# Kernel tuning notes

Hardware: AMD Instinct MI355X
Metric: run time of the kernel (lower is better)

## Reference

```python
import jax, jax.numpy as jnp
import numpy as np

H = 16        # attention heads
TOP_K = 2     # experts per token
EPS = 1e-5


def _layer_norm(x, g, b):
    m = x.mean(-1, keepdims=True)
    v = ((x - m) ** 2).mean(-1, keepdims=True)
    return (x - m) * jax.lax.rsqrt(v + EPS) * g + b


def setup_inputs() -> dict:
    key = jax.random.key(0)
    ks = jax.random.split(key, 12)
    B, S, D, F, E = 8, 512, 1024, 4096, 8
    inp = {
        "x": jax.random.normal(ks[0], (B, S, D), jnp.float32),
        "ln1_g": jnp.ones((D,), jnp.float32),
        "ln1_b": jnp.zeros((D,), jnp.float32),
        "ln2_g": jnp.ones((D,), jnp.float32),
        "ln2_b": jnp.zeros((D,), jnp.float32),
        "w_qkv": jax.random.normal(ks[1], (D, 3 * D), jnp.float32) * (D ** -0.5),
        "w_o": jax.random.normal(ks[2], (D, D), jnp.float32) * (D ** -0.5),
        "w_gate": jax.random.normal(ks[3], (D, E), jnp.float32) * (D ** -0.5),
        "w1": jax.random.normal(ks[4], (E, D, F), jnp.float32) * (D ** -0.5),
        "b1": jnp.zeros((E, F), jnp.float32),
        "w2": jax.random.normal(ks[5], (E, F, D), jnp.float32) * (F ** -0.5),
        "b2": jnp.zeros((E, D), jnp.float32),
    }
    return inp


def _block(x, ln1_g, ln1_b, ln2_g, ln2_b, w_qkv, w_o, w_gate, w1, b1, w2, b2):
    B, S, D = x.shape
    hd = D // H
    # --- attention (causal MHA) ---
    h = _layer_norm(x, ln1_g, ln1_b)
    qkv = h @ w_qkv                                   # [B,S,3D]
    q, k, v = jnp.split(qkv, 3, axis=-1)
    q = q.reshape(B, S, H, hd)
    k = k.reshape(B, S, H, hd)
    v = v.reshape(B, S, H, hd)
    scores = jnp.einsum("bqhd,bkhd->bhqk", q, k) * (hd ** -0.5)
    causal = jnp.tril(jnp.ones((S, S), bool))
    scores = jnp.where(causal, scores, jnp.finfo(scores.dtype).min)
    attn = jax.nn.softmax(scores, axis=-1)
    o = jnp.einsum("bhqk,bkhd->bqhd", attn, v).reshape(B, S, D)
    x_resid = x + o @ w_o
    # --- MoE FFN (top-k routing; dispatch/expert/combine math) ---
    moe_in = _layer_norm(x_resid, ln2_g, ln2_b)
    N = B * S
    xf = moe_in.reshape(N, D)
    probs = jax.nn.softmax(xf @ w_gate, axis=-1)       # [N,E]
    top_w, top_i = jax.lax.top_k(probs, TOP_K)         # [N,K]
    top_w = top_w / top_w.sum(-1, keepdims=True)       # renormalize over chosen experts
    E = w1.shape[0]
    out = jnp.zeros_like(xf)
    for e in range(E):                                 # fixed small expert loop
        gate_e = jnp.sum(jnp.where(top_i == e, top_w, 0.0), axis=-1)  # [N] combine weight
        he = jax.nn.gelu(xf @ w1[e] + b1[e])           # [N,F]
        out = out + gate_e[:, None] * (he @ w2[e] + b2[e])
    return out.reshape(B, S, D) + x_resid


def reference(x, ln1_g, ln1_b, ln2_g, ln2_b, w_qkv, w_o, w_gate, w1, b1, w2, b2):
    return _block(x, ln1_g, ln1_b, ln2_g, ln2_b, w_qkv, w_o, w_gate, w1, b1, w2, b2)
```

## Files before the change

kernel.cpp:

```cpp
#include <hip/hip_runtime.h>

#define DEV static __device__ __forceinline__

typedef __bf16 bf16;
typedef __bf16 bf16x8 __attribute__((ext_vector_type(8)));
typedef float f32x4 __attribute__((ext_vector_type(4)));

static_assert(sizeof(bf16x8) == 16, "bf16x8 must be 16B");

DEV void gll16(const void* g, void* l) {
  __builtin_amdgcn_global_load_lds(
      (const __attribute__((address_space(1))) unsigned int*)g,
      (__attribute__((address_space(3))) unsigned int*)l, 16, 0, 0);
}

__global__ void transpose_cvt_kernel(const float* __restrict__ src, bf16* __restrict__ hi,
                                     bf16* __restrict__ lo, int R, int C) {
  __shared__ float t[32][33];
  const int z = blockIdx.z;
  const size_t zoff = (size_t)z * R * C;
  const int c0 = blockIdx.x * 32, r0 = blockIdx.y * 32;
  const int tid = threadIdx.x;
#pragma unroll
  for (int i = 0; i < 4; ++i) {
    int idx = tid + i * 256;
    int r = idx >> 5, c = idx & 31;
    t[r][c] = src[zoff + (size_t)(r0 + r) * C + (c0 + c)];
  }
  __syncthreads();
#pragma unroll
  for (int i = 0; i < 4; ++i) {
    int idx = tid + i * 256;
    int c = idx >> 5, r = idx & 31;
    float v = t[r][c];
    bf16 h = (bf16)v;
    size_t o = zoff + (size_t)(c0 + c) * R + (r0 + r);
    hi[o] = h;
    if (lo) lo[o] = (bf16)(v - (float)h);
  }
}

DEV void block_reduce2(float& a, float& b, float* red, int tid) {
#pragma unroll
  for (int m = 32; m >= 1; m >>= 1) {
    a += __shfl_xor(a, m);
    b += __shfl_xor(b, m);
  }
  if ((tid & 63) == 0) {
    red[(tid >> 6) * 2] = a;
    red[(tid >> 6) * 2 + 1] = b;
  }
  __syncthreads();
  a = red[0] + red[2] + red[4] + red[6];
  b = red[1] + red[3] + red[5] + red[7];
}

__global__ void ln_split_kernel(const float* __restrict__ x, const float* __restrict__ g,
                                const float* __restrict__ bb, bf16* __restrict__ hi,
                                bf16* __restrict__ lo) {
  __shared__ float red[8];
  const int n = blockIdx.x, tid = threadIdx.x;
  const float* row = x + (size_t)n * 1024;
  float4 v = *(const float4*)(row + tid * 4);
  float s = v.x + v.y + v.z + v.w;
  float ss = v.x * v.x + v.y * v.y + v.z * v.z + v.w * v.w;
  block_reduce2(s, ss, red, tid);
  float mean = s * (1.f / 1024.f);
  float var = ss * (1.f / 1024.f) - mean * mean;
  float rstd = rsqrtf(var + 1e-5f);
  float vv[4] = {v.x, v.y, v.z, v.w};
#pragma unroll
  for (int c = 0; c < 4; ++c) {
    int col = tid * 4 + c;
    float y = (vv[c] - mean) * rstd * g[col] + bb[col];
    bf16 h = (bf16)y;
    size_t o = (size_t)n * 1024 + col;
    hi[o] = h;
    lo[o] = (bf16)(y - (float)h);
  }
}

__global__ __launch_bounds__(256, 2) void gemm_x3_kernel(
    const bf16* __restrict__ Ah, const bf16* __restrict__ Al, const bf16* __restrict__ Bh,
    const bf16* __restrict__ Bl, const float* __restrict__ addend, float* __restrict__ C, int M,
    int N, int K) {
  __shared__ bf16 As_h[128 * 64];
  __shared__ bf16 As_l[128 * 64];
  __shared__ bf16 Bs_h[128 * 64];
  __shared__ bf16 Bs_l[128 * 64];
  const int tid = threadIdx.x;
  const int w = tid >> 6, lane = tid & 63;
  const int quad = lane >> 4, l15 = lane & 15;
  const int m0 = blockIdx.y * 128, n0 = blockIdx.x * 128;
  const int wm = (w >> 1) * 64, wn = (w & 1) * 64;
  const int r8 = lane >> 3, c8 = lane & 7;

  size_t gA[4], gB[4];
  unsigned lbase[4];
#pragma unroll
  for (int i = 0; i < 4; ++i) {
    int rr = ((w * 4 + i) << 3) + r8;
    gA[i] = (size_t)(m0 + rr) * K + (c8 << 3);
    gB[i] = (size_t)(n0 + rr) * K + (c8 << 3);
    lbase[i] = (unsigned)((w * 4 + i) << 9);
  }
  const f32x4 fz = {0.f, 0.f, 0.f, 0.f};
  f32x4 acc[4][4];
#pragma unroll
  for (int a = 0; a < 4; ++a)
#pragma unroll
    for (int b = 0; b < 4; ++b) acc[a][b] = fz;

  for (int k0 = 0; k0 < K; k0 += 64) {
#pragma unroll
    for (int i = 0; i < 4; ++i) {
      gll16(Ah + gA[i] + k0, As_h + lbase[i]);
      gll16(Al + gA[i] + k0, As_l + lbase[i]);
      gll16(Bh + gB[i] + k0, Bs_h + lbase[i]);
      gll16(Bl + gB[i] + k0, Bs_l + lbase[i]);
    }
    __syncthreads();
#pragma unroll
    for (int ks = 0; ks < 2; ++ks) {
      bf16x8 a_h[4], a_l[4], b_h[4], b_l[4];
#pragma unroll
      for (int mi = 0; mi < 4; ++mi) {
        int off = (wm + mi * 16 + l15) * 64 + ks * 32 + quad * 8;
        a_h[mi] = *(const bf16x8*)(As_h + off);
        a_l[mi] = *(const bf16x8*)(As_l + off);
      }
#pragma unroll
      for (int ni = 0; ni < 4; ++ni) {
        int off = (wn + ni * 16 + l15) * 64 + ks * 32 + quad * 8;
        b_h[ni] = *(const bf16x8*)(Bs_h + off);
        b_l[ni] = *(const bf16x8*)(Bs_l + off);
      }
#pragma unroll
      for (int mi = 0; mi < 4; ++mi)
#pragma unroll
        for (int ni = 0; ni < 4; ++ni) {
          acc[mi][ni] = __builtin_amdgcn_mfma_f32_16x16x32_bf16(a_h[mi], b_h[ni], acc[mi][ni], 0, 0, 0);
          acc[mi][ni] = __builtin_amdgcn_mfma_f32_16x16x32_bf16(a_h[mi], b_l[ni], acc[mi][ni], 0, 0, 0);
          acc[mi][ni] = __builtin_amdgcn_mfma_f32_16x16x32_bf16(a_l[mi], b_h[ni], acc[mi][ni], 0, 0, 0);
        }
    }
    __syncthreads();
  }
#pragma unroll
  for (int mi = 0; mi < 4; ++mi)
#pragma unroll
    for (int r = 0; r < 4; ++r) {
      int row = m0 + wm + mi * 16 + quad * 4 + r;
      size_t rb = (size_t)row * N;
#pragma unroll
      for (int ni = 0; ni < 4; ++ni) {
        int col = n0 + wn + ni * 16 + l15;
        float v = acc[mi][ni][r];
        if (addend) v += addend[rb + col];
        C[rb + col] = v;
      }
    }
}

__global__ __launch_bounds__(256) void attn_kernel(const float* __restrict__ qkv,
                                                   bf16* __restrict__ o_hi,
                                                   bf16* __restrict__ o_lo) {
  __shared__ float Ks[64][64];
  __shared__ float Vs[64][64];
  const int bh = blockIdx.x;
  const int b = bh >> 4, h = bh & 15;
  const int q0 = blockIdx.y * 64;
  const int tid = threadIdx.x;
  const int ql = tid >> 2, sub = tid & 3;
  const size_t rowq = (size_t)(b * 512 + q0 + ql) * 3072 + h * 64 + sub * 16;
  float q[16];
#pragma unroll
  for (int j = 0; j < 16; ++j) q[j] = qkv[rowq + j] * 0.125f;
  float m_i = -1e30f, l_i = 0.f;
  float o[16];
#pragma unroll
  for (int j = 0; j < 16; ++j) o[j] = 0.f;
  const int ntiles = blockIdx.y + 1;
  for (int t = 0; t < ntiles; ++t) {
    const int kv0 = t * 64;
    __syncthreads();
    for (int i = tid; i < 1024; i += 256) {
      int r = i >> 4, c4 = (i & 15) << 2;
      const float* kp = qkv + (size_t)(b * 512 + kv0 + r) * 3072 + 1024 + h * 64 + c4;
      *(float4*)&Ks[r][c4] = *(const float4*)kp;
      *(float4*)&Vs[r][c4] = *(const float4*)(kp + 1024);
    }
    __syncthreads();
    const int kvlim = min(64, q0 + ql - kv0 + 1);
    for (int kv = 0; kv < kvlim; ++kv) {
      float s = 0.f;
#pragma unroll
      for (int j = 0; j < 16; ++j) s += q[j] * Ks[kv][sub * 16 + j];
      s += __shfl_xor(s, 1);
      s += __shfl_xor(s, 2);
      float m_new = fmaxf(m_i, s);
      float alpha = __expf(m_i - m_new);
      float p = __expf(s - m_new);
      l_i = l_i * alpha + p;
#pragma unroll
      for (int j = 0; j < 16; ++j) o[j] = o[j] * alpha + p * Vs[kv][sub * 16 + j];
      m_i = m_new;
    }
  }
  const float inv = 1.f / l_i;
  const size_t ob = (size_t)(b * 512 + q0 + ql) * 1024 + h * 64 + sub * 16;
#pragma unroll
  for (int j = 0; j < 16; ++j) {
    float v = o[j] * inv;
    bf16 hh = (bf16)v;
    o_hi[ob + j] = hh;
    o_lo[ob + j] = (bf16)(v - (float)hh);
  }
}

__global__ void ln2_gate_kernel(const float* __restrict__ xr, const float* __restrict__ g,
                                const float* __restrict__ bb, const float* __restrict__ wg,
                                bf16* __restrict__ moe_b, float* __restrict__ top_w,
                                int* __restrict__ top_i, int* __restrict__ counts) {
  __shared__ float red[8];
  __shared__ float red8[4][8];
  const int n = blockIdx.x, tid = threadIdx.x;
  const float* row = xr + (size_t)n * 1024;
  float4 v = *(const float4*)(row + tid * 4);
  float s = v.x + v.y + v.z + v.w;
  float ss = v.x * v.x + v.y * v.y + v.z * v.z + v.w * v.w;
  block_reduce2(s, ss, red, tid);
  float mean = s * (1.f / 1024.f);
  float var = ss * (1.f / 1024.f) - mean * mean;
  float rstd = rsqrtf(var + 1e-5f);
  float vv[4] = {v.x, v.y, v.z, v.w};
  float a8[8];
#pragma unroll
  for (int e = 0; e < 8; ++e) a8[e] = 0.f;
#pragma unroll
  for (int c = 0; c < 4; ++c) {
    int col = tid * 4 + c;
    float y = (vv[c] - mean) * rstd * g[col] + bb[col];
    moe_b[(size_t)n * 1024 + col] = (bf16)y;
    const float* wr = wg + (size_t)col * 8;
#pragma unroll
    for (int e = 0; e < 8; ++e) a8[e] += y * wr[e];
  }
#pragma unroll
  for (int e = 0; e < 8; ++e)
#pragma unroll
    for (int m = 32; m >= 1; m >>= 1) a8[e] += __shfl_xor(a8[e], m);
  if ((tid & 63) == 0)
#pragma unroll
    for (int e = 0; e < 8; ++e) red8[tid >> 6][e] = a8[e];
  __syncthreads();
  if (tid == 0) {
    float lg[8];
#pragma unroll
    for (int e = 0; e < 8; ++e) lg[e] = red8[0][e] + red8[1][e] + red8[2][e] + red8[3][e];
    float mx = lg[0];
#pragma unroll
    for (int e = 1; e < 8; ++e) mx = fmaxf(mx, lg[e]);
    float pe[8];
#pragma unroll
    for (int e = 0; e < 8; ++e) pe[e] = __expf(lg[e] - mx);
    int i1 = 0;
    float p1 = pe[0];
#pragma unroll
    for (int e = 1; e < 8; ++e)
      if (pe[e] > p1) { p1 = pe[e]; i1 = e; }
    int i2 = -1;
    float p2 = -1.f;
#pragma unroll
    for (int e = 0; e < 8; ++e)
      if (e != i1 && pe[e] > p2) { p2 = pe[e]; i2 = e; }
    float inv = 1.f / (p1 + p2);
    top_w[n * 2] = p1 * inv;
    top_w[n * 2 + 1] = p2 * inv;
    top_i[n * 2] = i1;
    top_i[n * 2 + 1] = i2;
    atomicAdd(&counts[i1], 1);
    atomicAdd(&counts[i2], 1);
  }
}

__global__ void offsets_kernel(const int* __restrict__ counts, int* __restrict__ offs) {
  if (threadIdx.x == 0 && blockIdx.x == 0) {
    int a = 0;
    for (int e = 0; e < 8; ++e) {
      offs[e] = a;
      a += counts[e];
    }
  }
}

__global__ void scatter_kernel(const int* __restrict__ top_i, const int* __restrict__ offs,
                               int* __restrict__ cursor, int* __restrict__ expert_tok,
                               int* __restrict__ inv_slot) {
  int n = blockIdx.x * 256 + threadIdx.x;
  if (n >= 4096) return;
#pragma unroll
  for (int k = 0; k < 2; ++k) {
    int e = top_i[n * 2 + k];
    int pos = atomicAdd(&cursor[e], 1);
    int slot = offs[e] + pos;
    expert_tok[slot] = n;
    inv_slot[n * 2 + k] = slot;
  }
}

DEV float gelu_tanh(float x) {
  float x3 = x * x * x;
  float t = tanhf(0.7978845608028654f * (x + 0.044715f * x3));
  return 0.5f * x * (1.f + t);
}

template <int GELU>
__global__ __launch_bounds__(256, 2) void gemm_moe_kernel(
    const bf16* __restrict__ A, const bf16* __restrict__ B, const float* __restrict__ bias,
    const int* __restrict__ counts, const int* __restrict__ offs, const int* __restrict__ gather,
    bf16* __restrict__ Out, int N, int K) {
  __shared__ bf16 As[128 * 64];
  __shared__ bf16 Bs[128 * 64];
  const int e = blockIdx.z;
  const int rows = counts[e];
  const int m0 = blockIdx.y * 128;
  if (m0 >= rows) return;
  const int off = offs[e];
  const int tid = threadIdx.x;
  const int w = tid >> 6, lane = tid & 63;
  const int quad = lane >> 4, l15 = lane & 15;
  const int n0 = blockIdx.x * 128;
  const int wm = (w >> 1) * 64, wn = (w & 1) * 64;
  const int r8 = lane >> 3, c8 = lane & 7;

  size_t gA[4], gB[4];
  unsigned lbase[4];
  const size_t bexp = (size_t)e * N * K;
#pragma unroll
  for (int i = 0; i < 4; ++i) {
    int rr = ((w * 4 + i) << 3) + r8;
    int lr = min(m0 + rr, rows - 1);
    int arow = gather ? gather[off + lr] : (off + lr);
    gA[i] = (size_t)arow * K + (c8 << 3);
    gB[i] = bexp + (size_t)(n0 + rr) * K + (c8 << 3);
    lbase[i] = (unsigned)((w * 4 + i) << 9);
  }
  const f32x4 fz = {0.f, 0.f, 0.f, 0.f};
  f32x4 acc[4][4];
#pragma unroll
  for (int a = 0; a < 4; ++a)
#pragma unroll
    for (int b = 0; b < 4; ++b) acc[a][b] = fz;

  for (int k0 = 0; k0 < K; k0 += 64) {
#pragma unroll
    for (int i = 0; i < 4; ++i) {
      gll16(A + gA[i] + k0, As + lbase[i]);
      gll16(B + gB[i] + k0, Bs + lbase[i]);
    }
    __syncthreads();
#pragma unroll
    for (int ks = 0; ks < 2; ++ks) {
      bf16x8 af[4], bf_[4];
#pragma unroll
      for (int mi = 0; mi < 4; ++mi)
        af[mi] = *(const bf16x8*)(As + (wm + mi * 16 + l15) * 64 + ks * 32 + quad * 8);
#pragma unroll
      for (int ni = 0; ni < 4; ++ni)
        bf_[ni] = *(const bf16x8*)(Bs + (wn + ni * 16 + l15) * 64 + ks * 32 + quad * 8);
#pragma unroll
      for (int mi = 0; mi < 4; ++mi)
#pragma unroll
        for (int ni = 0; ni < 4; ++ni)
          acc[mi][ni] = __builtin_amdgcn_mfma_f32_16x16x32_bf16(af[mi], bf_[ni], acc[mi][ni], 0, 0, 0);
    }
    __syncthreads();
  }
#pragma unroll
  for (int mi = 0; mi < 4; ++mi)
#pragma unroll
    for (int r = 0; r < 4; ++r) {
      int lrow = wm + mi * 16 + quad * 4 + r;
      int grow = m0 + lrow;
      if (grow < rows) {
        size_t ob = (size_t)(off + grow) * N;
#pragma unroll
        for (int ni = 0; ni < 4; ++ni) {
          int col = n0 + wn + ni * 16 + l15;
          float v = acc[mi][ni][r] + bias[(size_t)e * N + col];
          if (GELU) v = gelu_tanh(v);
          Out[ob + col] = (bf16)v;
        }
      }
    }
}

__global__ void combine_kernel(const float* __restrict__ xr, const bf16* __restrict__ y,
                               const float* __restrict__ top_w, const int* __restrict__ inv_slot,
                               float* __restrict__ out) {
  const int n = blockIdx.x, tid = threadIdx.x;
  const float w0 = top_w[n * 2], w1 = top_w[n * 2 + 1];
  const size_t s0 = (size_t)inv_slot[n * 2] * 1024;
  const size_t s1 = (size_t)inv_slot[n * 2 + 1] * 1024;
  const int c = tid * 4;
  const size_t base = (size_t)n * 1024 + c;
  float4 xv = *(const float4*)(xr + base);
  const bf16* y0 = y + s0 + c;
  const bf16* y1 = y + s1 + c;
  float4 o;
  o.x = xv.x + w0 * (float)y0[0] + w1 * (float)y1[0];
  o.y = xv.y + w0 * (float)y0[1] + w1 * (float)y1[1];
  o.z = xv.z + w0 * (float)y0[2] + w1 * (float)y1[2];
  o.w = xv.w + w0 * (float)y0[3] + w1 * (float)y1[3];
  *(float4*)(out + base) = o;
}

extern "C" void kernel_launch(void* const* d_in, const int* in_sizes, int n_in, void* d_out,
                              int out_size, void* d_ws, size_t ws_size, hipStream_t stream) {
  const float* x = (const float*)d_in[0];
  const float* ln1_g = (const float*)d_in[1];
  const float* ln1_b = (const float*)d_in[2];
  const float* ln2_g = (const float*)d_in[3];
  const float* ln2_b = (const float*)d_in[4];
  const float* w_qkv = (const float*)d_in[5];
  const float* w_o = (const float*)d_in[6];
  const float* w_gate = (const float*)d_in[7];
  const float* w1 = (const float*)d_in[8];
  const float* b1 = (const float*)d_in[9];
  const float* w2 = (const float*)d_in[10];
  const float* b2 = (const float*)d_in[11];
  float* out = (float*)d_out;

  char* p = (char*)d_ws;
  auto take = [&](size_t bytes) {
    char* r = p;
    p += (bytes + 255) & ~(size_t)255;
    return r;
  };
  bf16* wqkvT_h = (bf16*)take((size_t)3072 * 1024 * 2);
  bf16* wqkvT_l = (bf16*)take((size_t)3072 * 1024 * 2);
  bf16* woT_h = (bf16*)take((size_t)1024 * 1024 * 2);
  bf16* woT_l = (bf16*)take((size_t)1024 * 1024 * 2);
  bf16* w1T = (bf16*)take((size_t)8 * 4096 * 1024 * 2);
  bf16* w2T = (bf16*)take((size_t)8 * 1024 * 4096 * 2);
  char* regionA = take(67108864);
  bf16* h_hi = (bf16*)regionA;
  bf16* h_lo = (bf16*)(regionA + 8388608);
  float* qkv = (float*)(regionA + 16777216);
  bf16* he = (bf16*)regionA;
  char* regionB = take(16777216);
  bf16* o_hi = (bf16*)regionB;
  bf16* o_lo = (bf16*)(regionB + 8388608);
  bf16* yb = (bf16*)regionB;
  float* x_resid = (float*)take((size_t)4096 * 1024 * 4);
  bf16* moe_b = (bf16*)take((size_t)4096 * 1024 * 2);
  float* top_w = (float*)take(4096 * 2 * 4);
  int* top_i = (int*)take(4096 * 2 * 4);
  int* counts = (int*)take(256);
  int* offs = (int*)take(256);
  int* cursor = (int*)take(256);
  int* expert_tok = (int*)take(8192 * 4);
  int* inv_slot = (int*)take(8192 * 4);

  hipMemsetAsync(counts, 0, 768, stream);

  transpose_cvt_kernel<<<dim3(96, 32, 1), 256, 0, stream>>>(w_qkv, wqkvT_h, wqkvT_l, 1024, 3072);
  transpose_cvt_kernel<<<dim3(32, 32, 1), 256, 0, stream>>>(w_o, woT_h, woT_l, 1024, 1024);
  transpose_cvt_kernel<<<dim3(128, 32, 8), 256, 0, stream>>>(w1, w1T, nullptr, 1024, 4096);
  transpose_cvt_kernel<<<dim3(32, 128, 8), 256, 0, stream>>>(w2, w2T, nullptr, 4096, 1024);

  ln_split_kernel<<<4096, 256, 0, stream>>>(x, ln1_g, ln1_b, h_hi, h_lo);
  gemm_x3_kernel<<<dim3(24, 32, 1), 256, 0, stream>>>(h_hi, h_lo, wqkvT_h, wqkvT_l, nullptr, qkv,
                                                      4096, 3072, 1024);
  attn_kernel<<<dim3(128, 8, 1), 256, 0, stream>>>(qkv, o_hi, o_lo);
  gemm_x3_kernel<<<dim3(8, 32, 1), 256, 0, stream>>>(o_hi, o_lo, woT_h, woT_l, x, x_resid, 4096,
                                                     1024, 1024);
  ln2_gate_kernel<<<4096, 256, 0, stream>>>(x_resid, ln2_g, ln2_b, w_gate, moe_b, top_w, top_i,
                                            counts);
  offsets_kernel<<<1, 64, 0, stream>>>(counts, offs);
  scatter_kernel<<<16, 256, 0, stream>>>(top_i, offs, cursor, expert_tok, inv_slot);
  gemm_moe_kernel<1><<<dim3(32, 32, 8), 256, 0, stream>>>(moe_b, w1T, b1, counts, offs, expert_tok,
                                                          he, 4096, 1024);
  gemm_moe_kernel<0><<<dim3(8, 32, 8), 256, 0, stream>>>(he, w2T, b2, counts, offs, nullptr, yb,
                                                         1024, 4096);
  combine_kernel<<<4096, 256, 0, stream>>>(x_resid, yb, top_w, inv_slot, out);
}
```

Baseline: 1.122 ms.

## Rewrite causal attention with split-bf16 MFMA flash kernel and KV prep pass

Replaces the scalar per-thread online-softmax attention with a flash-style kernel that computes QK^T and PV using 16x16x32 bf16 MFMA. Each operand is split into hi/lo bf16 pairs to preserve near-fp32 accuracy. A new prep kernel converts K to hi/lo bf16 and transposes V once per tile, so attention can stream tiles into LDS with global_load_lds. Query tiles are scheduled longest-first, and the prep buffers alias the memory later used for x_resid and moe_b. This adds an extra launch and a four-term MFMA cost in exchange for removing the scalar FP32 dot-product and accumulate loops.

```diff
diff --git a/kernel.cpp b/kernel.cpp
--- a/kernel.cpp
+++ b/kernel.cpp
@@ -3,10 +3,13 @@
 #define DEV static __device__ __forceinline__
 
 typedef __bf16 bf16;
+typedef __bf16 bf16x4 __attribute__((ext_vector_type(4)));
 typedef __bf16 bf16x8 __attribute__((ext_vector_type(8)));
 typedef float f32x4 __attribute__((ext_vector_type(4)));
 
 static_assert(sizeof(bf16x8) == 16, "bf16x8 must be 16B");
+
+#define MFMA16(a, b, c) __builtin_amdgcn_mfma_f32_16x16x32_bf16((a), (b), (c), 0, 0, 0)
 
 DEV void gll16(const void* g, void* l) {
   __builtin_amdgcn_global_load_lds(
@@ -139,9 +142,9 @@
       for (int mi = 0; mi < 4; ++mi)
 #pragma unroll
         for (int ni = 0; ni < 4; ++ni) {
-          acc[mi][ni] = __builtin_amdgcn_mfma_f32_16x16x32_bf16(a_h[mi], b_h[ni], acc[mi][ni], 0, 0, 0);
-          acc[mi][ni] = __builtin_amdgcn_mfma_f32_16x16x32_bf16(a_h[mi], b_l[ni], acc[mi][ni], 0, 0, 0);
-          acc[mi][ni] = __builtin_amdgcn_mfma_f32_16x16x32_bf16(a_l[mi], b_h[ni], acc[mi][ni], 0, 0, 0);
+          acc[mi][ni] = MFMA16(a_h[mi], b_h[ni], acc[mi][ni]);
+          acc[mi][ni] = MFMA16(a_h[mi], b_l[ni], acc[mi][ni]);
+          acc[mi][ni] = MFMA16(a_l[mi], b_h[ni], acc[mi][ni]);
         }
     }
     __syncthreads();
@@ -162,59 +165,191 @@
     }
 }
 
-__global__ __launch_bounds__(256) void attn_kernel(const float* __restrict__ qkv,
-                                                   bf16* __restrict__ o_hi,
-                                                   bf16* __restrict__ o_lo) {
-  __shared__ float Ks[64][64];
-  __shared__ float Vs[64][64];
-  const int bh = blockIdx.x;
+__global__ __launch_bounds__(256) void kv_prep_kernel(const float* __restrict__ qkv,
+                                                      bf16* __restrict__ Kh, bf16* __restrict__ Kl,
+                                                      bf16* __restrict__ Vh, bf16* __restrict__ Vl) {
+  __shared__ float vt[64 * 65];
+  const int blk = blockIdx.x, tid = threadIdx.x;
+  const int bh = blk >> 3, t = blk & 7;
   const int b = bh >> 4, h = bh & 15;
-  const int q0 = blockIdx.y * 64;
+  const size_t tile = (size_t)blk * 4096;
+#pragma unroll
+  for (int it = 0; it < 4; ++it) {
+    int fi = tid + it * 256;
+    int r = fi >> 4, c4 = (fi & 15) << 2;
+    const float* src = qkv + (size_t)(b * 512 + t * 64 + r) * 3072 + 1024 + h * 64 + c4;
+    float4 kk4 = *(const float4*)src;
+    float4 vv4 = *(const float4*)(src + 1024);
+    float kk[4] = {kk4.x, kk4.y, kk4.z, kk4.w};
+    float vv[4] = {vv4.x, vv4.y, vv4.z, vv4.w};
+    bf16x4 h4, l4;
+#pragma unroll
+    for (int j = 0; j < 4; ++j) {
+      bf16 hh = (bf16)kk[j];
+      h4[j] = hh;
+      l4[j] = (bf16)(kk[j] - (float)hh);
+    }
+    *(bf16x4*)(Kh + tile + r * 64 + c4) = h4;
+    *(bf16x4*)(Kl + tile + r * 64 + c4) = l4;
+#pragma unroll
+    for (int j = 0; j < 4; ++j) vt[r * 65 + c4 + j] = vv[j];
+  }
+  __syncthreads();
+#pragma unroll
+  for (int it = 0; it < 4; ++it) {
+    int fi = tid + it * 256;
+    int d = fi >> 4, k4 = (fi & 15) << 2;
+    bf16x4 h4, l4;
+#pragma unroll
+    for (int j = 0; j < 4; ++j) {
+      float v = vt[(k4 + j) * 65 + d];
+      bf16 hh = (bf16)v;
+      h4[j] = hh;
+      l4[j] = (bf16)(v - (float)hh);
+    }
+    *(bf16x4*)(Vh + tile + d * 64 + k4) = h4;
+    *(bf16x4*)(Vl + tile + d * 64 + k4) = l4;
+  }
+}
+
+__global__ __launch_bounds__(256, 3) void attn_mfma_kernel(
+    const float* __restrict__ qkv, const bf16* __restrict__ Kh, const bf16* __restrict__ Kl,
+    const bf16* __restrict__ Vh, const bf16* __restrict__ Vl, bf16* __restrict__ o_hi,
+    bf16* __restrict__ o_lo) {
+  __shared__ bf16 Ks_h[4096], Ks_l[4096], Vs_h[4096], Vs_l[4096];
+  __shared__ bf16 Ps_h[64 * 68], Ps_l[64 * 68];
   const int tid = threadIdx.x;
-  const int ql = tid >> 2, sub = tid & 3;
-  const size_t rowq = (size_t)(b * 512 + q0 + ql) * 3072 + h * 64 + sub * 16;
-  float q[16];
-#pragma unroll
-  for (int j = 0; j < 16; ++j) q[j] = qkv[rowq + j] * 0.125f;
-  float m_i = -1e30f, l_i = 0.f;
-  float o[16];
-#pragma unroll
-  for (int j = 0; j < 16; ++j) o[j] = 0.f;
-  const int ntiles = blockIdx.y + 1;
-  for (int t = 0; t < ntiles; ++t) {
-    const int kv0 = t * 64;
+  const int w = tid >> 6, lane = tid & 63, quad = lane >> 4, l15 = lane & 15;
+  const int bh = blockIdx.x & 127, qt = 7 - (blockIdx.x >> 7);
+  const int b = bh >> 4, h = bh & 15;
+
+  bf16x8 q_h[2], q_l[2];
+  {
+    const int qrow = b * 512 + qt * 64 + w * 16 + l15;
+#pragma unroll
+    for (int ks = 0; ks < 2; ++ks) {
+      const float* src = qkv + (size_t)qrow * 3072 + h * 64 + ks * 32 + quad * 8;
+      float4 v0 = *(const float4*)src, v1 = *(const float4*)(src + 4);
+      float vv[8] = {v0.x, v0.y, v0.z, v0.w, v1.x, v1.y, v1.z, v1.w};
+#pragma unroll
+      for (int j = 0; j < 8; ++j) {
+        float q = vv[j] * 0.125f;
+        bf16 hh = (bf16)q;
+        q_h[ks][j] = hh;
+        q_l[ks][j] = (bf16)(q - (float)hh);
+      }
+    }
+  }
+  float m_r[4] = {-1e30f, -1e30f, -1e30f, -1e30f};
+  float l_r[4] = {0.f, 0.f, 0.f, 0.f};
+  const f32x4 fz = {0.f, 0.f, 0.f, 0.f};
+  f32x4 acc[4] = {fz, fz, fz, fz};
+  const size_t tb0 = (size_t)bh * 8 * 4096;
+
+  for (int t = 0; t <= qt; ++t) {
     __syncthreads();
-    for (int i = tid; i < 1024; i += 256) {
-      int r = i >> 4, c4 = (i & 15) << 2;
-      const float* kp = qkv + (size_t)(b * 512 + kv0 + r) * 3072 + 1024 + h * 64 + c4;
-      *(float4*)&Ks[r][c4] = *(const float4*)kp;
-      *(float4*)&Vs[r][c4] = *(const float4*)(kp + 1024);
+    {
+      const size_t g = tb0 + (size_t)t * 4096;
+#pragma unroll
+      for (int i = 0; i < 2; ++i) {
+        const int off = (w * 2 + i) << 9;
+        gll16(Kh + g + off + lane * 8, Ks_h + off);
+        gll16(Kl + g + off + lane * 8, Ks_l + off);
+        gll16(Vh + g + off + lane * 8, Vs_h + off);
+        gll16(Vl + g + off + lane * 8, Vs_l + off);
+      }
     }
     __syncthreads();
-    const int kvlim = min(64, q0 + ql - kv0 + 1);
-    for (int kv = 0; kv < kvlim; ++kv) {
-      float s = 0.f;
-#pragma unroll
-      for (int j = 0; j < 16; ++j) s += q[j] * Ks[kv][sub * 16 + j];
-      s += __shfl_xor(s, 1);
-      s += __shfl_xor(s, 2);
-      float m_new = fmaxf(m_i, s);
-      float alpha = __expf(m_i - m_new);
-      float p = __expf(s - m_new);
-      l_i = l_i * alpha + p;
-#pragma unroll
-      for (int j = 0; j < 16; ++j) o[j] = o[j] * alpha + p * Vs[kv][sub * 16 + j];
-      m_i = m_new;
-    }
-  }
-  const float inv = 1.f / l_i;
-  const size_t ob = (size_t)(b * 512 + q0 + ql) * 1024 + h * 64 + sub * 16;
-#pragma unroll
-  for (int j = 0; j < 16; ++j) {
-    float v = o[j] * inv;
-    bf16 hh = (bf16)v;
-    o_hi[ob + j] = hh;
-    o_lo[ob + j] = (bf16)(v - (float)hh);
+    f32x4 s[4];
+#pragma unroll
+    for (int nt = 0; nt < 4; ++nt) {
+      s[nt] = fz;
+#pragma unroll
+      for (int ks = 0; ks < 2; ++ks) {
+        const int ko = (nt * 16 + l15) * 64 + ks * 32 + quad * 8;
+        bf16x8 kh = *(const bf16x8*)(Ks_h + ko);
+        bf16x8 kl = *(const bf16x8*)(Ks_l + ko);
+        s[nt] = MFMA16(q_h[ks], kh, s[nt]);
+        s[nt] = MFMA16(q_h[ks], kl, s[nt]);
+        s[nt] = MFMA16(q_l[ks], kh, s[nt]);
+        s[nt] = MFMA16(q_l[ks], kl, s[nt]);
+      }
+    }
+    if (t == qt) {
+      const int qlr = w * 16 + quad * 4;
+#pragma unroll
+      for (int nt = 0; nt < 4; ++nt) {
+        const int kvl = nt * 16 + l15;
+#pragma unroll
+        for (int r = 0; r < 4; ++r)
+          if (kvl > qlr + r) s[nt][r] = -1e30f;
+      }
+    }
+#pragma unroll
+    for (int r = 0; r < 4; ++r) {
+      float mx = fmaxf(fmaxf(s[0][r], s[1][r]), fmaxf(s[2][r], s[3][r]));
+      mx = fmaxf(mx, __shfl_xor(mx, 1));
+      mx = fmaxf(mx, __shfl_xor(mx, 2));
+      mx = fmaxf(mx, __shfl_xor(mx, 4));
+      mx = fmaxf(mx, __shfl_xor(mx, 8));
+      const float mnew = fmaxf(m_r[r], mx);
+      const float alpha = __expf(m_r[r] - mnew);
+      m_r[r] = mnew;
+      float rs = 0.f;
+      const int pbase = (w * 16 + quad * 4 + r) * 68 + l15;
+#pragma unroll
+      for (int nt = 0; nt < 4; ++nt) {
+        float p = __expf(s[nt][r] - mnew);
+        rs += p;
+        bf16 ph = (bf16)p;
+        Ps_h[pbase + nt * 16] = ph;
+        Ps_l[pbase + nt * 16] = (bf16)(p - (float)ph);
+      }
+      rs += __shfl_xor(rs, 1);
+      rs += __shfl_xor(rs, 2);
+      rs += __shfl_xor(rs, 4);
+      rs += __shfl_xor(rs, 8);
+      l_r[r] = l_r[r] * alpha + rs;
+#pragma unroll
+      for (int nt = 0; nt < 4; ++nt) acc[nt][r] *= alpha;
+    }
+#pragma unroll
+    for (int ks = 0; ks < 2; ++ks) {
+      const int pb = (w * 16 + l15) * 68 + ks * 32 + quad * 8;
+      bf16x4 ph0 = *(const bf16x4*)(Ps_h + pb), ph1 = *(const bf16x4*)(Ps_h + pb + 4);
+      bf16x4 pl0 = *(const bf16x4*)(Ps_l + pb), pl1 = *(const bf16x4*)(Ps_l + pb + 4);
+      bf16x8 pf_h, pf_l;
+#pragma unroll
+      for (int j = 0; j < 4; ++j) {
+        pf_h[j] = ph0[j];
+        pf_h[4 + j] = ph1[j];
+        pf_l[j] = pl0[j];
+        pf_l[4 + j] = pl1[j];
+      }
+#pragma unroll
+      for (int nt = 0; nt < 4; ++nt) {
+        const int vo = (nt * 16 + l15) * 64 + ks * 32 + quad * 8;
+        bf16x8 vh = *(const bf16x8*)(Vs_h + vo);
+        bf16x8 vl = *(const bf16x8*)(Vs_l + vo);
+        acc[nt] = MFMA16(pf_h, vh, acc[nt]);
+        acc[nt] = MFMA16(pf_h, vl, acc[nt]);
+        acc[nt] = MFMA16(pf_l, vh, acc[nt]);
+        acc[nt] = MFMA16(pf_l, vl, acc[nt]);
+      }
+    }
+  }
+  const int orow0 = b * 512 + qt * 64 + w * 16 + quad * 4;
+#pragma unroll
+  for (int r = 0; r < 4; ++r) {
+    const float inv = 1.f / l_r[r];
+    const size_t ob = (size_t)(orow0 + r) * 1024 + h * 64 + l15;
+#pragma unroll
+    for (int nt = 0; nt < 4; ++nt) {
+      float v = acc[nt][r] * inv;
+      bf16 hh = (bf16)v;
+      o_hi[ob + nt * 16] = hh;
+      o_lo[ob + nt * 16] = (bf16)(v - (float)hh);
+    }
   }
 }
 
@@ -372,8 +507,7 @@
 #pragma unroll
       for (int mi = 0; mi < 4; ++mi)
 #pragma unroll
-        for (int ni = 0; ni < 4; ++ni)
-          acc[mi][ni] = __builtin_amdgcn_mfma_f32_16x16x32_bf16(af[mi], bf_[ni], acc[mi][ni], 0, 0, 0);
+        for (int ni = 0; ni < 4; ++ni) acc[mi][ni] = MFMA16(af[mi], bf_[ni], acc[mi][ni]);
     }
     __syncthreads();
   }
@@ -453,8 +587,13 @@
   bf16* o_hi = (bf16*)regionB;
   bf16* o_lo = (bf16*)(regionB + 8388608);
   bf16* yb = (bf16*)regionB;
-  float* x_resid = (float*)take((size_t)4096 * 1024 * 4);
-  bf16* moe_b = (bf16*)take((size_t)4096 * 1024 * 2);
+  char* regionC = take(33554432);
+  bf16* Kh = (bf16*)regionC;
+  bf16* Kl = (bf16*)(regionC + 8388608);
+  bf16* Vh = (bf16*)(regionC + 16777216);
+  bf16* Vl = (bf16*)(regionC + 25165824);
+  float* x_resid = (float*)regionC;
+  bf16* moe_b = (bf16*)(regionC + 16777216);
   float* top_w = (float*)take(4096 * 2 * 4);
   int* top_i = (int*)take(4096 * 2 * 4);
   int* counts = (int*)take(256);
@@ -473,7 +612,8 @@
   ln_split_kernel<<<4096, 256, 0, stream>>>(x, ln1_g, ln1_b, h_hi, h_lo);
   gemm_x3_kernel<<<dim3(24, 32, 1), 256, 0, stream>>>(h_hi, h_lo, wqkvT_h, wqkvT_l, nullptr, qkv,
                                                       4096, 3072, 1024);
-  attn_kernel<<<dim3(128, 8, 1), 256, 0, stream>>>(qkv, o_hi, o_lo);
+  kv_prep_kernel<<<1024, 256, 0, stream>>>(qkv, Kh, Kl, Vh, Vl);
+  attn_mfma_kernel<<<1024, 256, 0, stream>>>(qkv, Kh, Kl, Vh, Vl, o_hi, o_lo);
   gemm_x3_kernel<<<dim3(8, 32, 1), 256, 0, stream>>>(o_hi, o_lo, woT_h, woT_l, x, x_resid, 4096,
                                                      1024, 1024);
   ln2_gate_kernel<<<4096, 256, 0, stream>>>(x_resid, ln2_g, ln2_b, w_gate, moe_b, top_w, top_i,
```

Result: faster. 1.000 ms (-10.8%).
